# Kernel tuning notes

Hardware: AMD Instinct MI355X
Metric: run time of the kernel (lower is better)

## Reference

```python
import jax, jax.numpy as jnp
import numpy as np

T = 20
TAU1 = 1.0
TAU2 = 0.9
RESET = 0.0
NUM_CLASSES = 4


def setup_inputs() -> dict:
    key = jax.random.key(0)
    ks = jax.random.split(key, 6)
    B, C_in, L = 64, 12, 4096
    c1, c2, K = 64, 64, 3
    x = jax.random.normal(ks[0], (B, C_in, L, T), dtype=jnp.float32)
    conv1_w = jax.random.normal(ks[1], (c1, C_in, K), dtype=jnp.float32) / np.float32(np.sqrt(C_in * K))
    conv1_b = jnp.zeros((c1,), jnp.float32)
    conv2_w = jax.random.normal(ks[2], (c2, c1, K), dtype=jnp.float32) / np.float32(np.sqrt(c1 * K))
    conv2_b = jnp.zeros((c2,), jnp.float32)
    gain = jnp.float32(3.0)
    th1 = jnp.float32(0.02)
    th2 = jnp.float32(0.02)
    fc_w = jax.random.normal(ks[3], (NUM_CLASSES, c2), dtype=jnp.float32) / np.float32(np.sqrt(c2))
    fc_b = jnp.zeros((NUM_CLASSES,), jnp.float32)
    return {"x": x, "conv1_w": conv1_w, "conv1_b": conv1_b,
            "conv2_w": conv2_w, "conv2_b": conv2_b,
            "gain": gain, "th1": th1, "th2": th2,
            "fc_w": fc_w, "fc_b": fc_b}


def _conv1d(inp, w, b):
    # inp: [B, Cin, L]; w: [Cout, Cin, K]; 'same' padding for K=3
    pad = (w.shape[-1] // 2, w.shape[-1] // 2)
    y = jax.lax.conv_general_dilated(inp, w, window_strides=(1,), padding=[pad],
                                     dimension_numbers=("NCH", "OIH", "NCH"))
    return y + b[None, :, None]


def reference(x, conv1_w, conv1_b, conv2_w, conv2_b, gain, th1, th2, fc_w, fc_b):
    B, _, L, _ = x.shape
    c1 = conv1_w.shape[0]
    c2 = conv2_w.shape[0]
    dt = x.dtype
    xT = jnp.moveaxis(x, -1, 0)  # [T, B, Cin, L]

    v1_0 = jnp.zeros((B, c1, L), dt)
    v2_0 = jnp.zeros((B, c2, L), dt)
    acc0 = jnp.zeros((B, c2, L), dt)

    def step(carry, xt):
        v1, v2, acc = carry
        i1 = _conv1d(xt, conv1_w, conv1_b) * gain
        v1 = v1 + (i1 - v1) / TAU1
        s1 = (v1 >= th1).astype(dt)
        v1 = jnp.where(s1 > 0, jnp.asarray(RESET, dt), v1)
        i2 = _conv1d(s1, conv2_w, conv2_b) * gain
        v2 = v2 + (i2 - v2) / TAU2
        s2 = (v2 >= th2).astype(dt)
        v2 = jnp.where(s2 > 0, jnp.asarray(RESET, dt), v2)
        return (v1, v2, acc + s2), None

    (v1, v2, acc), _ = jax.lax.scan(step, (v1_0, v2_0, acc0), xT)
    out = acc / jnp.asarray(float(T), dt)        # [B, c2, L]
    pooled = jnp.mean(out, axis=-1)              # AdaptiveAvgPool1d(1) + squeeze -> [B, c2]
    logits = pooled @ fc_w.T + fc_b              # [B, NUM_CLASSES]
    return logits
```

## Files before the change

### kernel.cpp

```cpp
#include <hip/hip_runtime.h>

#define T_STEPS 20
#define NB      64
#define CIN     12
#define LLEN    4096
#define C1N     64
#define C2N     64
#define TL      64
#define NTHR    256
#define NT2     256
#define XR      68
#define NELEM   (CIN * XR)
#define NLD     4
#define XPR     70
#define XPP     56
#define S1ROWS  66
#define S1PITCH 72
#define TXL     256

#define W1T_OFF_F   0
#define POOL_OFF_F  2304
#define W2BF_OFF_B  25600
#define XT_OFF_B    (1u << 20)
#define XT_BYTES    ((size_t)NB * CIN * T_STEPS * LLEN * 4)
#define WS_NEED_B   ((size_t)XT_OFF_B + XT_BYTES)

using bf16x8 = __attribute__((ext_vector_type(8))) short;
using f32x4  = __attribute__((ext_vector_type(4))) float;

__device__ inline unsigned short f32_to_bf16_rne(float f) {
    unsigned u = __builtin_bit_cast(unsigned, f);
    return (unsigned short)((u + 0x7FFFu + ((u >> 16) & 1u)) >> 16);
}
__device__ inline float bf16f(unsigned short h) {
    return __builtin_bit_cast(float, (unsigned)h << 16);
}
__device__ inline void split3(float w, unsigned short& h, unsigned short& m, unsigned short& l) {
    h = f32_to_bf16_rne(w);
    float r1 = w - bf16f(h);
    m = f32_to_bf16_rne(r1);
    float r2 = r1 - bf16f(m);
    l = f32_to_bf16_rne(r2);
}

__global__ __launch_bounds__(NT2) void prep_weights(
    const float* __restrict__ w1, const float* __restrict__ w2,
    float* __restrict__ ws)
{
    int i = blockIdx.x * NT2 + threadIdx.x;
    float* w1t = ws + W1T_OFF_F;
    unsigned short* w2b = (unsigned short*)((char*)ws + W2BF_OFF_B);
    if (i < C1N * CIN * 3) {
        int c1 = i / (CIN * 3), r = i % (CIN * 3);
        w1t[r * C1N + c1] = w1[i];
    }
    if (i < C2N * C1N * 3) {
        int dk = i % 3, rem = i / 3;
        int ci = rem % C1N, c2 = rem / C1N;
        float w = w2[i];
        unsigned short hi = f32_to_bf16_rne(w);
        float hif = bf16f(hi);
        unsigned short lo = f32_to_bf16_rne(w - hif);
        w2b[((0 * 3 + dk) * C2N + c2) * C1N + ci] = hi;
        w2b[((1 * 3 + dk) * C2N + c2) * C1N + ci] = lo;
    }
}

__global__ __launch_bounds__(NT2) void transpose_x(
    const float* __restrict__ xg, float* __restrict__ xt)
{
    __shared__ float tile[TXL * 21];
    const int tid = threadIdx.x;
    const int l0  = blockIdx.x * TXL;
    const int bci = blockIdx.y;
    const float* src = xg + ((size_t)bci * LLEN + l0) * T_STEPS;
#pragma unroll
    for (int k = 0; k < TXL * T_STEPS / NT2; ++k) {
        int e = tid + k * NT2;
        tile[(e / T_STEPS) * 21 + (e % T_STEPS)] = src[e];
    }
    __syncthreads();
    float* dst = xt + (size_t)bci * T_STEPS * LLEN + l0;
#pragma unroll
    for (int t = 0; t < T_STEPS; ++t)
        dst[(size_t)t * LLEN + tid] = tile[tid * 21 + t];
}

__global__ __launch_bounds__(NTHR) void snn_main(
    const float* __restrict__ xg, const float* __restrict__ xt, int use_xt,
    const float* __restrict__ b1g, const float* __restrict__ b2g,
    const float* __restrict__ gp, const float* __restrict__ t1p,
    const float* __restrict__ t2p, const float* __restrict__ w1g,
    const float* __restrict__ ws, float* __restrict__ pooled)
{
    __shared__ __align__(16) float          xs32[2][NELEM];
    __shared__ __align__(16) unsigned short xsp[2][XPR][XPP];
    __shared__ __align__(16) unsigned short s1t[2][S1ROWS][S1PITCH];

    const int tid  = threadIdx.x;
    const int lane = tid & 63;
    const int wv   = __builtin_amdgcn_readfirstlane(tid >> 6);
    const int cb   = wv * 16;
    const int b    = blockIdx.y;
    const int l0   = blockIdx.x * TL;

    const float gain = gp[0], th1 = t1p[0], th2 = t2p[0];
    const unsigned short* __restrict__ w2b =
        (const unsigned short*)((const char*)ws + W2BF_OFF_B);

    const int m16 = lane & 15;
    const int q8  = ((lane >> 4) & 3) * 8;

    bf16x8 bw[2][3][2];
    {
        int c2 = cb + m16;
#pragma unroll
        for (int h = 0; h < 2; ++h)
#pragma unroll
            for (int dk = 0; dk < 3; ++dk)
#pragma unroll
                for (int cc = 0; cc < 2; ++cc)
                    bw[h][dk][cc] = *(const bf16x8*)
                        (w2b + (((h * 3 + dk) * C2N + c2) * C1N + cc * 32 + q8));
    }
    const float b2v = b2g[cb + m16];
    const float b1d = b1g[cb + m16];

    bf16x8 cw[3][2];
    {
        int co = cb + m16;
#pragma unroll
        for (int j = 0; j < 8; ++j) {
            int K = q8 + j;
            {
                int tap = K >> 4, ci = K & 15;
                float w = (ci < CIN) ? w1g[(co * CIN + ci) * 3 + tap] : 0.f;
                unsigned short h, m, l; split3(w, h, m, l);
                cw[0][0][j] = (short)h; cw[1][0][j] = (short)m; cw[2][0][j] = (short)l;
            }
            {
                float w = (K < CIN) ? w1g[(co * CIN + K) * 3 + 2] : 0.f;
                unsigned short h, m, l; split3(w, h, m, l);
                cw[0][1][j] = (short)h; cw[1][1][j] = (short)m; cw[2][1][j] = (short)l;
            }
        }
    }

    float v2s[4][4], accs[4][4];
#pragma unroll
    for (int lt = 0; lt < 4; ++lt)
#pragma unroll
        for (int r = 0; r < 4; ++r) { v2s[lt][r] = 0.f; accs[lt][r] = 0.f; }

    for (int e = tid; e < 112 + 816; e += NTHR) {
        if (e < 112) {
            int buf = e / 56, rem = e % 56, row = 68 + rem / 28, dw = rem % 28;
            *(unsigned*)((char*)&xsp[buf][row][0] + dw * 4) = 0u;
        } else {
            int e2 = e - 112, br = e2 / 6, ds = e2 % 6;
            int buf = br / XR, row = br % XR, pl = ds >> 1, dw = ds & 1;
            *(unsigned*)((char*)&xsp[buf][row][0] + pl * 32 + 24 + dw * 4) = 0u;
        }
    }

    const float* __restrict__ srcp =
        use_xt ? (xt + (size_t)b * CIN * T_STEPS * LLEN)
               : (xg + (size_t)b * CIN * LLEN * T_STEPS);
    const unsigned tstep = use_xt ? (unsigned)LLEN : 1u;

    unsigned off[NLD];
    bool ldok[NLD], gok[NLD];
    float pf[NLD];
#pragma unroll
    for (int k = 0; k < NLD; ++k) {
        int i  = tid + k * NTHR;
        bool w = i < NELEM;
        int iv = w ? i : 0;
        int ci = iv / XR, rx = iv - ci * XR;
        int gl = l0 - 2 + rx;
        bool g = w && ((unsigned)gl < (unsigned)LLEN);
        int glc = g ? gl : 0;
        off[k]  = use_xt ? (unsigned)(ci * T_STEPS * LLEN + glc)
                         : (unsigned)((ci * LLEN + glc) * T_STEPS);
        ldok[k] = w; gok[k] = g;
    }
    float* __restrict__ xf0 = &xs32[0][0];
    float* __restrict__ xf1 = &xs32[1][0];

    const bool t2z    = q8 >= 16;
    const int  aoff01 = (m16 + (t2z ? 1 : 0)) * 112 + (q8 & 8) * 2;
    const int  aoff2  = (m16 + 2) * 112 + (q8 & 8) * 2;
    const int  zoff   = 68 * 112 + (q8 & 8) * 2;

#pragma unroll
    for (int k = 0; k < NLD; ++k) pf[k] = gok[k] ? srcp[off[k]] : 0.f;
#pragma unroll
    for (int k = 0; k < NLD; ++k) if (ldok[k]) xf0[tid + k * NTHR] = pf[k];
#pragma unroll
    for (int k = 0; k < NLD; ++k) pf[k] = gok[k] ? srcp[off[k] + tstep] : 0.f;
    __syncthreads();
#pragma unroll
    for (int k = 0; k < NLD; ++k) {
        int e = tid + k * NTHR;
        if (e < NELEM) {
            int rx = e / CIN, ci = e - rx * CIN;
            unsigned short h, m, l; split3(xs32[0][ci * XR + rx], h, m, l);
            xsp[0][rx][ci] = h; xsp[0][rx][16 + ci] = m; xsp[0][rx][32 + ci] = l;
        }
    }
#pragma unroll
    for (int k = 0; k < NLD; ++k) if (ldok[k]) xf1[tid + k * NTHR] = pf[k];
#pragma unroll
    for (int k = 0; k < NLD; ++k)
        pf[k] = gok[k] ? srcp[off[k] + 2u * tstep] : 0.f;
    __syncthreads();

#pragma unroll 1
    for (int tt = 0; tt <= T_STEPS; ++tt) {
        if (tt > 0) {
            const unsigned short (*__restrict__ s1p)[S1PITCH] = s1t[(tt - 1) & 1];
#pragma unroll
            for (int lt = 0; lt < 4; ++lt) {
                f32x4 d = {0.f, 0.f, 0.f, 0.f};
#pragma unroll
                for (int dk = 0; dk < 3; ++dk) {
                    int row = lt * 16 + m16 + dk;
#pragma unroll
                    for (int cc = 0; cc < 2; ++cc) {
                        bf16x8 a = *(const bf16x8*)&s1p[row][cc * 32 + q8];
                        d = __builtin_amdgcn_mfma_f32_16x16x32_bf16(a, bw[0][dk][cc], d, 0, 0, 0);
                        d = __builtin_amdgcn_mfma_f32_16x16x32_bf16(a, bw[1][dk][cc], d, 0, 0, 0);
                    }
                }
#pragma unroll
                for (int r = 0; r < 4; ++r) {
                    float i2 = (d[r] + b2v) * gain;
                    float v  = v2s[lt][r] + (i2 - v2s[lt][r]) * (1.0f / 0.9f);
                    bool  sp = v >= th2;
                    v2s[lt][r]   = sp ? 0.f : v;
                    accs[lt][r] += sp ? 1.f : 0.f;
                }
            }
        }

        if (tt < T_STEPS) {
            unsigned short (*__restrict__ s1c)[S1PITCH] = s1t[tt & 1];
            const char* xp = (const char*)&xsp[tt & 1][0][0];
#pragma unroll
            for (int ti = 0; ti < 5; ++ti) {
                const int tb = (ti < 4) ? ti * 16 : 52;
                const char* base01 = xp + tb * 112 + aoff01;
                const char* base2  = t2z ? (xp + zoff) : (xp + tb * 112 + aoff2);
                bf16x8 ah01 = *(const bf16x8*)(base01 + 0);
                bf16x8 am01 = *(const bf16x8*)(base01 + 32);
                bf16x8 al01 = *(const bf16x8*)(base01 + 64);
                bf16x8 ah2  = *(const bf16x8*)(base2 + 0);
                bf16x8 am2  = *(const bf16x8*)(base2 + 32);
                bf16x8 al2  = *(const bf16x8*)(base2 + 64);
                f32x4 d = {b1d, b1d, b1d, b1d};
                d = __builtin_amdgcn_mfma_f32_16x16x32_bf16(ah01, cw[0][0], d, 0, 0, 0);
                d = __builtin_amdgcn_mfma_f32_16x16x32_bf16(ah2,  cw[0][1], d, 0, 0, 0);
                d = __builtin_amdgcn_mfma_f32_16x16x32_bf16(ah01, cw[1][0], d, 0, 0, 0);
                d = __builtin_amdgcn_mfma_f32_16x16x32_bf16(ah2,  cw[1][1], d, 0, 0, 0);
                d = __builtin_amdgcn_mfma_f32_16x16x32_bf16(am01, cw[0][0], d, 0, 0, 0);
                d = __builtin_amdgcn_mfma_f32_16x16x32_bf16(am2,  cw[0][1], d, 0, 0, 0);
                d = __builtin_amdgcn_mfma_f32_16x16x32_bf16(ah01, cw[2][0], d, 0, 0, 0);
                d = __builtin_amdgcn_mfma_f32_16x16x32_bf16(ah2,  cw[2][1], d, 0, 0, 0);
                d = __builtin_amdgcn_mfma_f32_16x16x32_bf16(al01, cw[0][0], d, 0, 0, 0);
                d = __builtin_amdgcn_mfma_f32_16x16x32_bf16(al2,  cw[0][1], d, 0, 0, 0);
                d = __builtin_amdgcn_mfma_f32_16x16x32_bf16(am01, cw[1][0], d, 0, 0, 0);
                d = __builtin_amdgcn_mfma_f32_16x16x32_bf16(am2,  cw[1][1], d, 0, 0, 0);
#pragma unroll
                for (int r = 0; r < 4; ++r) {
                    int m  = ((lane >> 4) & 3) * 4 + r;
                    int rs = tb + m;
                    bool keep  = (ti < 4) || (m == 12 || m == 13);
                    bool valid = (unsigned)(l0 - 1 + rs) < (unsigned)LLEN;
                    bool sp    = valid && (d[r] * gain >= th1);
                    if (keep)
                        s1c[rs][cb + m16] = sp ? (unsigned short)0x3F80u : (unsigned short)0u;
                }
            }
        }

        if (tt + 1 < T_STEPS) {
            const int nb = (tt + 1) & 1;
#pragma unroll
            for (int k = 0; k < NLD; ++k) {
                int e = tid + k * NTHR;
                if (e < NELEM) {
                    int rx = e / CIN, ci = e - rx * CIN;
                    unsigned short h, m, l; split3(xs32[nb][ci * XR + rx], h, m, l);
                    xsp[nb][rx][ci] = h; xsp[nb][rx][16 + ci] = m; xsp[nb][rx][32 + ci] = l;
                }
            }
        }
        if (tt + 2 < T_STEPS) {
            float* __restrict__ xn = (tt & 1) ? xf1 : xf0;
#pragma unroll
            for (int k = 0; k < NLD; ++k)
                if (ldok[k]) xn[tid + k * NTHR] = pf[k];
        }
        if (tt + 3 < T_STEPS) {
#pragma unroll
            for (int k = 0; k < NLD; ++k)
                pf[k] = gok[k] ? srcp[off[k] + (size_t)(tt + 3) * tstep] : 0.f;
        }
        __syncthreads();
    }

    float s = 0.f;
#pragma unroll
    for (int lt = 0; lt < 4; ++lt)
#pragma unroll
        for (int r = 0; r < 4; ++r) s += accs[lt][r];
    s += __shfl_down(s, 32, 64);
    s += __shfl_down(s, 16, 64);
    if (lane < 16) atomicAdd(&pooled[b * C2N + cb + lane], s);
}

__global__ __launch_bounds__(NT2) void fc_kernel(
    const float* __restrict__ pooled, const float* __restrict__ fcw,
    const float* __restrict__ fcb, float* __restrict__ out)
{
    int i = threadIdx.x, b = i >> 2, cls = i & 3;
    float s = 0.f;
#pragma unroll 8
    for (int c = 0; c < C2N; ++c)
        s += pooled[b * C2N + c] * fcw[cls * C2N + c];
    out[b * 4 + cls] = s * (1.0f / ((float)T_STEPS * (float)LLEN)) + fcb[cls];
}

extern "C" void kernel_launch(void* const* d_in, const int* in_sizes, int n_in,
                              void* d_out, int out_size, void* d_ws, size_t ws_size,
                              hipStream_t stream)
{
    const float* xg  = (const float*)d_in[0];
    const float* w1  = (const float*)d_in[1];
    const float* b1  = (const float*)d_in[2];
    const float* w2  = (const float*)d_in[3];
    const float* b2  = (const float*)d_in[4];
    const float* gp  = (const float*)d_in[5];
    const float* t1  = (const float*)d_in[6];
    const float* t2  = (const float*)d_in[7];
    const float* fcw = (const float*)d_in[8];
    const float* fcb = (const float*)d_in[9];
    float* ws  = (float*)d_ws;
    float* out = (float*)d_out;

    const int use_xt = (ws_size >= WS_NEED_B) ? 1 : 0;
    float* xt = (float*)((char*)d_ws + XT_OFF_B);

    hipMemsetAsync(ws + POOL_OFF_F, 0, NB * C2N * sizeof(float), stream);
    prep_weights<<<(C2N * C1N * 3 + NT2 - 1) / NT2, NT2, 0, stream>>>(w1, w2, ws);
    if (use_xt)
        transpose_x<<<dim3(LLEN / TXL, NB * CIN), NT2, 0, stream>>>(xg, xt);
    snn_main<<<dim3(LLEN / TL, NB), NTHR, 0, stream>>>(xg, xt, use_xt,
                                                       b1, b2, gp, t1, t2, w1,
                                                       ws, ws + POOL_OFF_F);
    fc_kernel<<<1, NT2, 0, stream>>>(ws + POOL_OFF_F, fcw, fcb, out);
}
```

Baseline: 925.4 us.

## Drop the x transpose pass and load channel pairs directly into packed bf16 LDS

Removes the separate transpose_x kernel and its extra read and write of the full input through workspace. The main kernel now reads x in its original [B,C,L,T] layout, with each thread handling a pair of channels at one position. It splits the values into bf16 hi/mid/lo and writes packed 32-bit words straight into the MFMA operand buffer, which drops the fp32 LDS staging buffer. The split-and-store and prefetch are moved ahead of the MFMA work, prefetch depth goes from three steps to two, and waves_per_eu(3) is added. The direct loads use a 20-float stride along L, so coalescing is worse and each step's load may be exposed to more latency.

```diff
diff --git a/kernel.cpp b/kernel.cpp
--- a/kernel.cpp
+++ b/kernel.cpp
@@ -10,20 +10,15 @@
 #define NTHR    256
 #define NT2     256
 #define XR      68
-#define NELEM   (CIN * XR)
-#define NLD     4
+#define NPAIR   (XR * 6)
+#define CITP    (LLEN * T_STEPS)
 #define XPR     70
 #define XPP     56
 #define S1ROWS  66
 #define S1PITCH 72
-#define TXL     256
-
-#define W1T_OFF_F   0
+
 #define POOL_OFF_F  2304
 #define W2BF_OFF_B  25600
-#define XT_OFF_B    (1u << 20)
-#define XT_BYTES    ((size_t)NB * CIN * T_STEPS * LLEN * 4)
-#define WS_NEED_B   ((size_t)XT_OFF_B + XT_BYTES)
 
 using bf16x8 = __attribute__((ext_vector_type(8))) short;
 using f32x4  = __attribute__((ext_vector_type(4))) float;
@@ -44,16 +39,10 @@
 }
 
 __global__ __launch_bounds__(NT2) void prep_weights(
-    const float* __restrict__ w1, const float* __restrict__ w2,
-    float* __restrict__ ws)
+    const float* __restrict__ w2, float* __restrict__ ws)
 {
     int i = blockIdx.x * NT2 + threadIdx.x;
-    float* w1t = ws + W1T_OFF_F;
     unsigned short* w2b = (unsigned short*)((char*)ws + W2BF_OFF_B);
-    if (i < C1N * CIN * 3) {
-        int c1 = i / (CIN * 3), r = i % (CIN * 3);
-        w1t[r * C1N + c1] = w1[i];
-    }
     if (i < C2N * C1N * 3) {
         int dk = i % 3, rem = i / 3;
         int ci = rem % C1N, c2 = rem / C1N;
@@ -66,34 +55,14 @@
     }
 }
 
-__global__ __launch_bounds__(NT2) void transpose_x(
-    const float* __restrict__ xg, float* __restrict__ xt)
-{
-    __shared__ float tile[TXL * 21];
-    const int tid = threadIdx.x;
-    const int l0  = blockIdx.x * TXL;
-    const int bci = blockIdx.y;
-    const float* src = xg + ((size_t)bci * LLEN + l0) * T_STEPS;
-#pragma unroll
-    for (int k = 0; k < TXL * T_STEPS / NT2; ++k) {
-        int e = tid + k * NT2;
-        tile[(e / T_STEPS) * 21 + (e % T_STEPS)] = src[e];
-    }
-    __syncthreads();
-    float* dst = xt + (size_t)bci * T_STEPS * LLEN + l0;
-#pragma unroll
-    for (int t = 0; t < T_STEPS; ++t)
-        dst[(size_t)t * LLEN + tid] = tile[tid * 21 + t];
-}
-
-__global__ __launch_bounds__(NTHR) void snn_main(
-    const float* __restrict__ xg, const float* __restrict__ xt, int use_xt,
+__global__ __launch_bounds__(NTHR) __attribute__((amdgpu_waves_per_eu(3)))
+void snn_main(
+    const float* __restrict__ xg,
     const float* __restrict__ b1g, const float* __restrict__ b2g,
     const float* __restrict__ gp, const float* __restrict__ t1p,
     const float* __restrict__ t2p, const float* __restrict__ w1g,
     const float* __restrict__ ws, float* __restrict__ pooled)
 {
-    __shared__ __align__(16) float          xs32[2][NELEM];
     __shared__ __align__(16) unsigned short xsp[2][XPR][XPP];
     __shared__ __align__(16) unsigned short s1t[2][S1ROWS][S1PITCH];
 
@@ -163,29 +132,24 @@
         }
     }
 
-    const float* __restrict__ srcp =
-        use_xt ? (xt + (size_t)b * CIN * T_STEPS * LLEN)
-               : (xg + (size_t)b * CIN * LLEN * T_STEPS);
-    const unsigned tstep = use_xt ? (unsigned)LLEN : 1u;
-
-    unsigned off[NLD];
-    bool ldok[NLD], gok[NLD];
-    float pf[NLD];
-#pragma unroll
-    for (int k = 0; k < NLD; ++k) {
-        int i  = tid + k * NTHR;
-        bool w = i < NELEM;
-        int iv = w ? i : 0;
-        int ci = iv / XR, rx = iv - ci * XR;
+    const float* __restrict__ srcp = xg + (size_t)b * CIN * CITP;
+    unsigned off2[2];
+    int      lds4[2];
+    bool     pok[2], gokp[2];
+    float    pf[2][2];
+#pragma unroll
+    for (int k = 0; k < 2; ++k) {
+        int e = tid + k * NTHR;
+        bool w = e < NPAIR;
+        int ev = w ? e : 0;
+        int rx = ev / 6, cp = ev - rx * 6;
         int gl = l0 - 2 + rx;
         bool g = w && ((unsigned)gl < (unsigned)LLEN);
         int glc = g ? gl : 0;
-        off[k]  = use_xt ? (unsigned)(ci * T_STEPS * LLEN + glc)
-                         : (unsigned)((ci * LLEN + glc) * T_STEPS);
-        ldok[k] = w; gok[k] = g;
-    }
-    float* __restrict__ xf0 = &xs32[0][0];
-    float* __restrict__ xf1 = &xs32[1][0];
+        off2[k] = (unsigned)(cp * 2 * CITP + glc * T_STEPS);
+        lds4[k] = rx * 112 + cp * 4;
+        pok[k] = w; gokp[k] = g;
+    }
 
     const bool t2z    = q8 >= 16;
     const int  aoff01 = (m16 + (t2z ? 1 : 0)) * 112 + (q8 & 8) * 2;
@@ -193,30 +157,52 @@
     const int  zoff   = 68 * 112 + (q8 & 8) * 2;
 
 #pragma unroll
-    for (int k = 0; k < NLD; ++k) pf[k] = gok[k] ? srcp[off[k]] : 0.f;
-#pragma unroll
-    for (int k = 0; k < NLD; ++k) if (ldok[k]) xf0[tid + k * NTHR] = pf[k];
-#pragma unroll
-    for (int k = 0; k < NLD; ++k) pf[k] = gok[k] ? srcp[off[k] + tstep] : 0.f;
-    __syncthreads();
-#pragma unroll
-    for (int k = 0; k < NLD; ++k) {
-        int e = tid + k * NTHR;
-        if (e < NELEM) {
-            int rx = e / CIN, ci = e - rx * CIN;
-            unsigned short h, m, l; split3(xs32[0][ci * XR + rx], h, m, l);
-            xsp[0][rx][ci] = h; xsp[0][rx][16 + ci] = m; xsp[0][rx][32 + ci] = l;
-        }
-    }
-#pragma unroll
-    for (int k = 0; k < NLD; ++k) if (ldok[k]) xf1[tid + k * NTHR] = pf[k];
-#pragma unroll
-    for (int k = 0; k < NLD; ++k)
-        pf[k] = gok[k] ? srcp[off[k] + 2u * tstep] : 0.f;
+    for (int k = 0; k < 2; ++k) {
+        pf[k][0] = gokp[k] ? srcp[off2[k]] : 0.f;
+        pf[k][1] = gokp[k] ? srcp[off2[k] + CITP] : 0.f;
+    }
+#pragma unroll
+    for (int k = 0; k < 2; ++k)
+        if (pok[k]) {
+            unsigned short h0, m0, e0, h1, m1, e1;
+            split3(pf[k][0], h0, m0, e0);
+            split3(pf[k][1], h1, m1, e1);
+            unsigned* bp = (unsigned*)((char*)&xsp[0][0][0] + lds4[k]);
+            bp[0]  = (unsigned)h0 | ((unsigned)h1 << 16);
+            bp[8]  = (unsigned)m0 | ((unsigned)m1 << 16);
+            bp[16] = (unsigned)e0 | ((unsigned)e1 << 16);
+        }
+#pragma unroll
+    for (int k = 0; k < 2; ++k) {
+        pf[k][0] = gokp[k] ? srcp[off2[k] + 1] : 0.f;
+        pf[k][1] = gokp[k] ? srcp[off2[k] + CITP + 1] : 0.f;
+    }
     __syncthreads();
 
 #pragma unroll 1
     for (int tt = 0; tt <= T_STEPS; ++tt) {
+        if (tt + 1 < T_STEPS) {
+            const int nb = (tt + 1) & 1;
+#pragma unroll
+            for (int k = 0; k < 2; ++k)
+                if (pok[k]) {
+                    unsigned short h0, m0, e0, h1, m1, e1;
+                    split3(pf[k][0], h0, m0, e0);
+                    split3(pf[k][1], h1, m1, e1);
+                    unsigned* bp = (unsigned*)((char*)&xsp[nb][0][0] + lds4[k]);
+                    bp[0]  = (unsigned)h0 | ((unsigned)h1 << 16);
+                    bp[8]  = (unsigned)m0 | ((unsigned)m1 << 16);
+                    bp[16] = (unsigned)e0 | ((unsigned)e1 << 16);
+                }
+        }
+        if (tt + 2 < T_STEPS) {
+#pragma unroll
+            for (int k = 0; k < 2; ++k) {
+                pf[k][0] = gokp[k] ? srcp[off2[k] + (unsigned)(tt + 2)] : 0.f;
+                pf[k][1] = gokp[k] ? srcp[off2[k] + CITP + (unsigned)(tt + 2)] : 0.f;
+            }
+        }
+
         if (tt > 0) {
             const unsigned short (*__restrict__ s1p)[S1PITCH] = s1t[(tt - 1) & 1];
 #pragma unroll
@@ -282,30 +268,6 @@
                 }
             }
         }
-
-        if (tt + 1 < T_STEPS) {
-            const int nb = (tt + 1) & 1;
-#pragma unroll
-            for (int k = 0; k < NLD; ++k) {
-                int e = tid + k * NTHR;
-                if (e < NELEM) {
-                    int rx = e / CIN, ci = e - rx * CIN;
-                    unsigned short h, m, l; split3(xs32[nb][ci * XR + rx], h, m, l);
-                    xsp[nb][rx][ci] = h; xsp[nb][rx][16 + ci] = m; xsp[nb][rx][32 + ci] = l;
-                }
-            }
-        }
-        if (tt + 2 < T_STEPS) {
-            float* __restrict__ xn = (tt & 1) ? xf1 : xf0;
-#pragma unroll
-            for (int k = 0; k < NLD; ++k)
-                if (ldok[k]) xn[tid + k * NTHR] = pf[k];
-        }
-        if (tt + 3 < T_STEPS) {
-#pragma unroll
-            for (int k = 0; k < NLD; ++k)
-                pf[k] = gok[k] ? srcp[off[k] + (size_t)(tt + 3) * tstep] : 0.f;
-        }
         __syncthreads();
     }
 
@@ -348,14 +310,9 @@
     float* ws  = (float*)d_ws;
     float* out = (float*)d_out;
 
-    const int use_xt = (ws_size >= WS_NEED_B) ? 1 : 0;
-    float* xt = (float*)((char*)d_ws + XT_OFF_B);
-
     hipMemsetAsync(ws + POOL_OFF_F, 0, NB * C2N * sizeof(float), stream);
-    prep_weights<<<(C2N * C1N * 3 + NT2 - 1) / NT2, NT2, 0, stream>>>(w1, w2, ws);
-    if (use_xt)
-        transpose_x<<<dim3(LLEN / TXL, NB * CIN), NT2, 0, stream>>>(xg, xt);
-    snn_main<<<dim3(LLEN / TL, NB), NTHR, 0, stream>>>(xg, xt, use_xt,
+    prep_weights<<<(C2N * C1N * 3 + NT2 - 1) / NT2, NT2, 0, stream>>>(w2, ws);
+    snn_main<<<dim3(LLEN / TL, NB), NTHR, 0, stream>>>(xg,
                                                        b1, b2, gp, t1, t2, w1,
                                                        ws, ws + POOL_OFF_F);
     fc_kernel<<<1, NT2, 0, stream>>>(ws + POOL_OFF_F, fcw, fcb, out);
```

Result: faster. 779.2 us (-15.8%).
